# Performance work log

Measured on AMD Instinct MI355X. Metric: run time of the kernel, lower is better.

The kernel has to match this reference:

```python
import jax, jax.numpy as jnp
import numpy as np

NUM_HEADS = 16
WINDOW_SIZE = 256  # config.window_size; layer is 'local'


def setup_inputs() -> dict:
    key = jax.random.key(0)
    ks = jax.random.split(key, 8)
    B, S, H = 4, 2048, 1024
    scale = 1.0 / np.sqrt(H)
    return {
        "x": jax.random.normal(ks[0], (B, S, H), dtype=jnp.float32),
        "x_clean": jax.random.normal(ks[1], (B, S, H), dtype=jnp.float32),
        "ablation_mask": jax.random.uniform(ks[2], (B, S, H), dtype=jnp.float32),
        "Wq": jax.random.normal(ks[3], (H, H), dtype=jnp.float32) * scale,
        "Wk": jax.random.normal(ks[4], (H, H), dtype=jnp.float32) * scale,
        "Wv": jax.random.normal(ks[5], (H, H), dtype=jnp.float32) * scale,
        "Wo": jax.random.normal(ks[6], (H, H), dtype=jnp.float32) * scale,
        "bo": jnp.zeros((H,), dtype=jnp.float32),
    }


def reference(x, x_clean, ablation_mask, Wq, Wk, Wv, Wo, bo):
    B, S, H = x.shape
    nh, hd = NUM_HEADS, H // NUM_HEADS

    def proj(inp, W):  # torch Linear: inp @ W.T -> split heads -> [B, nh, S, hd]
        return jnp.einsum('bsh,oh->bso', inp, W).reshape(B, S, nh, hd).transpose(0, 2, 1, 3)

    q = proj(x, Wq)
    k = proj(x_clean, Wk)
    v = proj(x_clean, Wv)

    # NOTE: original applies NO 1/sqrt(head_dim) scaling.
    scores = jnp.einsum('bnsd,bntd->bnst', q, k)  # [B, nh, S, S]

    i = jnp.arange(S)[:, None]
    j = jnp.arange(S)[None, :]
    # local mask: forbid future (j > i) OR too-far past (j <= i - window)
    masked = (j > i) | (j <= i - WINDOW_SIZE)
    scores = jnp.where(masked[None, None, :, :], -jnp.inf, scores)

    attn = jax.nn.softmax(scores, axis=-1)
    context = jnp.einsum('bnst,bntd->bnsd', attn, v)          # [B, nh, S, hd]
    context = context.transpose(0, 2, 1, 3).reshape(B, S, H)   # merge heads
    context = context * ablation_mask
    return jnp.einsum('bsh,oh->bso', context, Wo) + bo
```

## Files before the change

### kernel.cpp

```cpp
#include <hip/hip_runtime.h>
#include <hip/hip_bf16.h>
#include <cstddef>

#define SB 4
#define SS 2048
#define SH 1024
#define NH 16
#define HD 64
#define WIN 256

typedef __attribute__((ext_vector_type(8))) short bf16x8;
typedef __attribute__((ext_vector_type(8))) _Float16 f16x8;
typedef __attribute__((ext_vector_type(2))) __fp16 fp16v2;
typedef __attribute__((ext_vector_type(4))) float f32x4;

static __device__ __forceinline__ ushort2 pk_bf16(float a, float b) {
    __hip_bfloat162 h = __float22bfloat162_rn(make_float2(a, b));
    union { __hip_bfloat162 h2; ushort2 u2; } u;
    u.h2 = h;
    return u.u2;
}
static __device__ __forceinline__ unsigned short pk1(float a) {
    return pk_bf16(a, 0.f).x;
}

static __device__ __forceinline__ void async16(const void* gptr, void* lptr) {
    __builtin_amdgcn_global_load_lds(
        (const __attribute__((address_space(1))) unsigned int*)gptr,
        (__attribute__((address_space(3))) unsigned int*)lptr, 16, 0, 0);
}

__global__ __launch_bounds__(256) void cvt_all(
    const float* __restrict__ x,  const float* __restrict__ xc,
    const float* __restrict__ Wq, const float* __restrict__ Wk,
    const float* __restrict__ Wv, const float* __restrict__ Wo,
    _Float16* __restrict__ xh,  _Float16* __restrict__ xch,
    _Float16* __restrict__ Wqh, _Float16* __restrict__ Wkh,
    _Float16* __restrict__ Wvh, _Float16* __restrict__ Woh)
{
    const int I4 = SB * SS * SH / 4;
    const int W4 = SH * SH / 4;
    int idx = blockIdx.x * 256 + threadIdx.x;
    const float* src;
    _Float16* dst;
    int off;
    if (idx < I4) { src = x; dst = xh; off = idx; }
    else if (idx < 2 * I4) { src = xc; dst = xch; off = idx - I4; }
    else {
        int r = idx - 2 * I4;
        int wi = r >> 18;
        off = r & (W4 - 1);
        src = (wi == 0) ? Wq : (wi == 1) ? Wk : (wi == 2) ? Wv : Wo;
        dst = (wi == 0) ? Wqh : (wi == 1) ? Wkh : (wi == 2) ? Wvh : Woh;
    }
    float4 v = ((const float4*)src)[off];
    union { fp16v2 h[2]; uint2 u; } t;
    t.h[0] = __builtin_amdgcn_cvt_pkrtz(v.x, v.y);
    t.h[1] = __builtin_amdgcn_cvt_pkrtz(v.z, v.w);
    ((uint2*)dst)[off] = t.u;
}

__global__ __launch_bounds__(256) void gemm_qkv(
    const _Float16* __restrict__ xh, const _Float16* __restrict__ xch,
    const _Float16* __restrict__ Wqh, const _Float16* __restrict__ Wkh,
    const _Float16* __restrict__ Wvh,
    _Float16* __restrict__ Qh, _Float16* __restrict__ Kh,
    unsigned short* __restrict__ Vt)
{
    const int M = SB * SS, N = SH, K = SH;
    __shared__ __align__(16) unsigned short smem[2 * 128 * 64];
    _Float16* Ah = (_Float16*)smem;
    _Float16* Bh = (_Float16*)smem + 8192;

    const int z = blockIdx.z;
    const _Float16* A = (z == 0) ? xh : xch;
    const _Float16* W = (z == 0) ? Wqh : (z == 1) ? Wkh : Wvh;

    const int tid = threadIdx.x;
    const int m0 = blockIdx.x * 128;
    const int n0 = blockIdx.y * 128;
    const int wave = tid >> 6;
    const int lane = tid & 63;
    const int wm = (wave & 1) * 64;
    const int wn = (wave >> 1) * 64;
    const int lrow = lane & 15;
    const int lk8 = (lane >> 4) * 8;
    const int rq = (lane >> 4) * 4;

    f32x4 acc[4][4];
#pragma unroll
    for (int i = 0; i < 4; ++i)
#pragma unroll
        for (int j = 0; j < 4; ++j)
            acc[i][j] = (f32x4){0.f, 0.f, 0.f, 0.f};

    for (int k0 = 0; k0 < K; k0 += 64) {
        __syncthreads();
#pragma unroll
        for (int ki = 0; ki < 2; ++ki)
#pragma unroll
            for (int u = 0; u < 2; ++u) {
                int reg = u * 4 + wave;
                int slot = reg * 64 + lane;
                int row = slot >> 2;
                int k8 = (slot & 3) * 8;
                async16(A + (size_t)(m0 + row) * K + k0 + ki * 32 + k8,
                        Ah + ki * 4096 + reg * 512);
                async16(W + (size_t)(n0 + row) * K + k0 + ki * 32 + k8,
                        Bh + ki * 4096 + reg * 512);
            }
        __syncthreads();

#pragma unroll
        for (int ki = 0; ki < 2; ++ki) {
            f16x8 bf[4];
#pragma unroll
            for (int j = 0; j < 4; ++j)
                bf[j] = *(const f16x8*)&Bh[ki * 4096 + (wn + j * 16 + lrow) * 32 + lk8];
#pragma unroll
            for (int i = 0; i < 4; ++i) {
                f16x8 af = *(const f16x8*)&Ah[ki * 4096 + (wm + i * 16 + lrow) * 32 + lk8];
#pragma unroll
                for (int j = 0; j < 4; ++j)
                    acc[i][j] = __builtin_amdgcn_mfma_f32_16x16x32_f16(af, bf[j], acc[i][j], 0, 0, 0);
            }
        }
    }

    if (z < 2) {
        _Float16* C = (z == 0) ? Qh : Kh;
#pragma unroll
        for (int i = 0; i < 4; ++i) {
            int rbase = m0 + wm + i * 16 + rq;
#pragma unroll
            for (int j = 0; j < 4; ++j) {
                int col = n0 + wn + j * 16 + lrow;
#pragma unroll
                for (int r = 0; r < 4; ++r)
                    C[(size_t)(rbase + r) * N + col] = (_Float16)acc[i][j][r];
            }
        }
    } else {
        unsigned short* T = smem;
#pragma unroll
        for (int p = 0; p < 2; ++p) {
            __syncthreads();
            if (wn == p * 64) {
#pragma unroll
                for (int i = 0; i < 4; ++i) {
                    int mloc = wm + i * 16 + rq;
#pragma unroll
                    for (int j = 0; j < 4; ++j) {
                        int cl = j * 16 + lrow;
                        *(ushort4*)&T[cl * 136 + mloc] = make_ushort4(
                            pk1(acc[i][j][0]), pk1(acc[i][j][1]),
                            pk1(acc[i][j][2]), pk1(acc[i][j][3]));
                    }
                }
            }
            __syncthreads();
#pragma unroll
            for (int u = 0; u < 4; ++u) {
                int slot = u * 256 + tid;
                int cl = slot >> 4;
                int m8 = (slot & 15) * 8;
                *(uint4*)(Vt + (size_t)(n0 + p * 64 + cl) * M + m0 + m8) =
                    *(const uint4*)&T[cl * 136 + m8];
            }
        }
    }
}

__global__ __launch_bounds__(256) void gemm_o(
    const _Float16* __restrict__ A, const _Float16* __restrict__ W,
    const float* __restrict__ bias, float* __restrict__ C)
{
    const int M = SB * SS, N = SH, K = SH;
    __shared__ __align__(16) unsigned short smem[2 * 128 * 64];
    _Float16* Ah = (_Float16*)smem;
    _Float16* Bh = (_Float16*)smem + 8192;

    const int tid = threadIdx.x;
    const int m0 = blockIdx.x * 128;
    const int n0 = blockIdx.y * 128;
    const int wave = tid >> 6;
    const int lane = tid & 63;
    const int wm = (wave & 1) * 64;
    const int wn = (wave >> 1) * 64;
    const int lrow = lane & 15;
    const int lk8 = (lane >> 4) * 8;
    const int rq = (lane >> 4) * 4;

    f32x4 acc[4][4];
#pragma unroll
    for (int i = 0; i < 4; ++i)
#pragma unroll
        for (int j = 0; j < 4; ++j)
            acc[i][j] = (f32x4){0.f, 0.f, 0.f, 0.f};

    for (int k0 = 0; k0 < K; k0 += 64) {
        __syncthreads();
#pragma unroll
        for (int ki = 0; ki < 2; ++ki)
#pragma unroll
            for (int u = 0; u < 2; ++u) {
                int reg = u * 4 + wave;
                int slot = reg * 64 + lane;
                int row = slot >> 2;
                int k8 = (slot & 3) * 8;
                async16(A + (size_t)(m0 + row) * K + k0 + ki * 32 + k8,
                        Ah + ki * 4096 + reg * 512);
                async16(W + (size_t)(n0 + row) * K + k0 + ki * 32 + k8,
                        Bh + ki * 4096 + reg * 512);
            }
        __syncthreads();

#pragma unroll
        for (int ki = 0; ki < 2; ++ki) {
            f16x8 bf[4];
#pragma unroll
            for (int j = 0; j < 4; ++j)
                bf[j] = *(const f16x8*)&Bh[ki * 4096 + (wn + j * 16 + lrow) * 32 + lk8];
#pragma unroll
            for (int i = 0; i < 4; ++i) {
                f16x8 af = *(const f16x8*)&Ah[ki * 4096 + (wm + i * 16 + lrow) * 32 + lk8];
#pragma unroll
                for (int j = 0; j < 4; ++j)
                    acc[i][j] = __builtin_amdgcn_mfma_f32_16x16x32_f16(af, bf[j], acc[i][j], 0, 0, 0);
            }
        }
    }

#pragma unroll
    for (int i = 0; i < 4; ++i) {
        int rbase = m0 + wm + i * 16 + rq;
#pragma unroll
        for (int j = 0; j < 4; ++j) {
            int col = n0 + wn + j * 16 + lrow;
            float badd = bias[col];
#pragma unroll
            for (int r = 0; r < 4; ++r)
                C[(size_t)(rbase + r) * N + col] = acc[i][j][r] + badd;
        }
    }
}

__global__ __launch_bounds__(256) void attn4(
    const _Float16* Qg, const _Float16* __restrict__ Kg,
    const unsigned short* __restrict__ Vtg, const float* __restrict__ amask,
    _Float16* ctxg)
{
    __shared__ __align__(16) _Float16 K_s[2][2 * 64 * 32];
    __shared__ __align__(16) unsigned short V_s[2][2 * 64 * 32];
    __shared__ __align__(16) unsigned short P_s[4][32 * 72];

    const int t = threadIdx.x;
    const int wave = t >> 6, lane = t & 63;
    const int qb = blockIdx.x, h = blockIdx.y, b = blockIdx.z;
    const int t0 = qb * 128;
    const int wq = t0 + wave * 32;
    const int lrow = lane & 15;
    const int lk8 = (lane >> 4) * 8;
    const int rq = (lane >> 4) * 4;
    const int M = SB * SS;
    unsigned short* P = P_s[wave];

    f16x8 qf[2][2];
#pragma unroll
    for (int i = 0; i < 2; ++i)
#pragma unroll
        for (int ki = 0; ki < 2; ++ki)
            qf[i][ki] = *(const f16x8*)(Qg +
                (size_t)(b * SS + wq + i * 16 + lrow) * SH + h * HD + ki * 32 + lk8);

    f32x4 o[2][4];
    float lsum[2][4];
#pragma unroll
    for (int i = 0; i < 2; ++i)
#pragma unroll
        for (int j = 0; j < 4; ++j) o[i][j] = (f32x4){0.f, 0.f, 0.f, 0.f};
#pragma unroll
    for (int i = 0; i < 2; ++i)
#pragma unroll
        for (int r = 0; r < 4; ++r) lsum[i][r] = 0.f;

    int cl0 = t0 - (WIN - 1);
    cl0 = cl0 < 0 ? 0 : cl0;
    const int c_lo = cl0 >> 6;
    const int c_hi = (t0 >> 6) + 1;

    auto stage = [&](int c, int buf) {
        const int key0 = c * 64;
#pragma unroll
        for (int ki = 0; ki < 2; ++ki) {
            int slot = wave * 64 + lane;
            int row = slot >> 2;
            int e8 = (slot & 3) * 8;
            async16(Kg + (size_t)(b * SS + key0 + row) * SH + h * HD + ki * 32 + e8,
                    (_Float16*)K_s[buf] + ki * 2048 + wave * 512);
            async16(Vtg + (size_t)(h * HD + row) * M + b * SS + key0 + ki * 32 + e8,
                    (unsigned short*)V_s[buf] + ki * 2048 + wave * 512);
        }
    };

    stage(c_lo, c_lo & 1);
    __syncthreads();

    for (int c = c_lo; c <= c_hi; ++c) {
        const int cur = c & 1;
        if (c < c_hi) stage(c + 1, cur ^ 1);
        const int key0 = c * 64;
        if (key0 <= wq + 31 && key0 + 63 >= wq - (WIN - 1)) {
            const _Float16* Kc = (const _Float16*)K_s[cur];
            const unsigned short* Vc = (const unsigned short*)V_s[cur];

            f32x4 s[2][4];
#pragma unroll
            for (int i = 0; i < 2; ++i)
#pragma unroll
                for (int j = 0; j < 4; ++j) s[i][j] = (f32x4){0.f, 0.f, 0.f, 0.f};
#pragma unroll
            for (int ki = 0; ki < 2; ++ki)
#pragma unroll
                for (int j = 0; j < 4; ++j) {
                    f16x8 bh = *(const f16x8*)&Kc[ki * 2048 + (j * 16 + lrow) * 32 + lk8];
#pragma unroll
                    for (int i = 0; i < 2; ++i)
                        s[i][j] = __builtin_amdgcn_mfma_f32_16x16x32_f16(qf[i][ki], bh, s[i][j], 0, 0, 0);
                }

#pragma unroll
            for (int i = 0; i < 2; ++i)
#pragma unroll
                for (int j = 0; j < 4; ++j) {
                    int jg = key0 + j * 16 + lrow;
#pragma unroll
                    for (int r = 0; r < 4; ++r) {
                        int qg = wq + i * 16 + rq + r;
                        float p = (jg <= qg && jg > qg - WIN) ? __expf(s[i][j][r]) : 0.f;
                        lsum[i][r] += p;
                        P[(i * 16 + rq + r) * 72 + j * 16 + lrow] = pk1(p);
                    }
                }

#pragma unroll
            for (int ki = 0; ki < 2; ++ki) {
                bf16x8 pf[2];
#pragma unroll
                for (int i = 0; i < 2; ++i)
                    pf[i] = *(const bf16x8*)&P[(i * 16 + lrow) * 72 + ki * 32 + lk8];
#pragma unroll
                for (int j = 0; j < 4; ++j) {
                    bf16x8 vf = *(const bf16x8*)&Vc[ki * 2048 + (j * 16 + lrow) * 32 + lk8];
#pragma unroll
                    for (int i = 0; i < 2; ++i)
                        o[i][j] = __builtin_amdgcn_mfma_f32_16x16x32_bf16(pf[i], vf, o[i][j], 0, 0, 0);
                }
            }
        }
        __syncthreads();
    }

#pragma unroll
    for (int i = 0; i < 2; ++i)
#pragma unroll
        for (int r = 0; r < 4; ++r) {
#pragma unroll
            for (int m = 1; m < 16; m <<= 1)
                lsum[i][r] += __shfl_xor(lsum[i][r], m);
        }

    _Float16* Pf = (_Float16*)P;
#pragma unroll
    for (int i = 0; i < 2; ++i)
#pragma unroll
        for (int r = 0; r < 4; ++r) {
            float inv = 1.f / lsum[i][r];
#pragma unroll
            for (int j = 0; j < 4; ++j)
                Pf[(i * 16 + rq + r) * 72 + j * 16 + lrow] = (_Float16)(o[i][j][r] * inv);
        }
#pragma unroll
    for (int u = 0; u < 4; ++u) {
        int slot = u * 64 + lane;
        int ro = slot >> 3;
        int d8 = (slot & 7) * 8;
        f16x8 v = *(const f16x8*)&Pf[ro * 72 + d8];
        size_t g = (size_t)(b * SS + wq + ro) * SH + h * HD + d8;
        float4 ma = *(const float4*)(amask + g);
        float4 mb = *(const float4*)(amask + g + 4);
        f16x8 rs;
        rs[0] = (_Float16)((float)v[0] * ma.x);
        rs[1] = (_Float16)((float)v[1] * ma.y);
        rs[2] = (_Float16)((float)v[2] * ma.z);
        rs[3] = (_Float16)((float)v[3] * ma.w);
        rs[4] = (_Float16)((float)v[4] * mb.x);
        rs[5] = (_Float16)((float)v[5] * mb.y);
        rs[6] = (_Float16)((float)v[6] * mb.z);
        rs[7] = (_Float16)((float)v[7] * mb.w);
        *(f16x8*)(ctxg + g) = rs;
    }
}

extern "C" void kernel_launch(void* const* d_in, const int* in_sizes, int n_in,
                              void* d_out, int out_size, void* d_ws, size_t ws_size,
                              hipStream_t stream)
{
    const float* x     = (const float*)d_in[0];
    const float* xc    = (const float*)d_in[1];
    const float* amask = (const float*)d_in[2];
    const float* Wq    = (const float*)d_in[3];
    const float* Wk    = (const float*)d_in[4];
    const float* Wv    = (const float*)d_in[5];
    const float* Wo    = (const float*)d_in[6];
    const float* bo    = (const float*)d_in[7];
    float* out = (float*)d_out;

    const int M = SB * SS;
    const size_t BUF = (size_t)M * SH;
    const size_t WBUF = (size_t)SH * SH;
    _Float16* xh  = (_Float16*)d_ws;
    _Float16* xch = xh + BUF;
    _Float16* Qh  = xch + BUF;
    _Float16* Kh  = Qh + BUF;
    unsigned short* Vt = (unsigned short*)(Kh + BUF);
    _Float16* Wqh = (_Float16*)(Vt + BUF);
    _Float16* Wkh = Wqh + WBUF;
    _Float16* Wvh = Wkh + WBUF;
    _Float16* Woh = Wvh + WBUF;
    _Float16* ctx = Qh;

    const int total4 = 2 * (M * SH / 4) + 4 * (SH * SH / 4);
    hipLaunchKernelGGL(cvt_all, dim3(total4 / 256), dim3(256), 0, stream,
                       x, xc, Wq, Wk, Wv, Wo, xh, xch, Wqh, Wkh, Wvh, Woh);

    hipLaunchKernelGGL(gemm_qkv, dim3(M / 128, SH / 128, 3), dim3(256), 0, stream,
                       xh, xch, Wqh, Wkh, Wvh, Qh, Kh, Vt);

    hipLaunchKernelGGL(attn4, dim3(SS / 128, NH, SB), dim3(256), 0, stream,
                       Qh, Kh, Vt, amask, ctx);

    hipLaunchKernelGGL(gemm_o, dim3(M / 128, SH / 128), dim3(256), 0, stream,
                       ctx, Woh, bo, out);
}
```

Baseline: 288.6 us.

## Stage Q/K GEMM output through LDS and widen attention blocks to 256 queries

The Q/K projection epilogue now writes the accumulators into an LDS tile and then stores them to global memory as coalesced 16-byte rows, replacing scattered 2-byte stores. The attention kernel moves to 512-thread blocks covering 256 queries, each with 8 waves, on a flattened 1D grid ordered so blocks with the same query tile across heads and batches launch together. Each staged K/V chunk is now shared by twice as many query rows, which cuts redundant window loads. In exchange each block loops over more chunks that some waves skip, and fewer blocks are launched.

Measured after the change: 276.8 us. 4.1% less time.

```diff
diff --git a/kernel.cpp b/kernel.cpp
--- a/kernel.cpp
+++ b/kernel.cpp
@@ -68,7 +68,7 @@
     unsigned short* __restrict__ Vt)
 {
     const int M = SB * SS, N = SH, K = SH;
-    __shared__ __align__(16) unsigned short smem[2 * 128 * 64];
+    __shared__ __align__(16) unsigned short smem[128 * 136];
     _Float16* Ah = (_Float16*)smem;
     _Float16* Bh = (_Float16*)smem + 8192;
 
@@ -129,16 +129,27 @@
 
     if (z < 2) {
         _Float16* C = (z == 0) ? Qh : Kh;
+        _Float16* T = (_Float16*)smem;
+        __syncthreads();
 #pragma unroll
         for (int i = 0; i < 4; ++i) {
-            int rbase = m0 + wm + i * 16 + rq;
+            int rloc = wm + i * 16 + rq;
 #pragma unroll
             for (int j = 0; j < 4; ++j) {
-                int col = n0 + wn + j * 16 + lrow;
+                int cl = wn + j * 16 + lrow;
 #pragma unroll
                 for (int r = 0; r < 4; ++r)
-                    C[(size_t)(rbase + r) * N + col] = (_Float16)acc[i][j][r];
-            }
+                    T[(rloc + r) * 136 + cl] = (_Float16)acc[i][j][r];
+            }
+        }
+        __syncthreads();
+#pragma unroll
+        for (int u = 0; u < 8; ++u) {
+            int slot = u * 256 + tid;
+            int row = slot >> 4;
+            int c8 = (slot & 15) * 8;
+            *(uint4*)(C + (size_t)(m0 + row) * N + n0 + c8) =
+                *(const uint4*)&T[row * 136 + c8];
         }
     } else {
         unsigned short* T = smem;
@@ -245,19 +256,22 @@
     }
 }
 
-__global__ __launch_bounds__(256) void attn4(
+__global__ __launch_bounds__(512, 4) void attn5(
     const _Float16* Qg, const _Float16* __restrict__ Kg,
     const unsigned short* __restrict__ Vtg, const float* __restrict__ amask,
     _Float16* ctxg)
 {
     __shared__ __align__(16) _Float16 K_s[2][2 * 64 * 32];
     __shared__ __align__(16) unsigned short V_s[2][2 * 64 * 32];
-    __shared__ __align__(16) unsigned short P_s[4][32 * 72];
+    __shared__ __align__(16) unsigned short P_s[8][32 * 72];
 
     const int t = threadIdx.x;
     const int wave = t >> 6, lane = t & 63;
-    const int qb = blockIdx.x, h = blockIdx.y, b = blockIdx.z;
-    const int t0 = qb * 128;
+    const int id = blockIdx.x;
+    const int qb = id >> 6;
+    const int pr = id & 63;
+    const int h = pr & 15, b = pr >> 4;
+    const int t0 = qb * 256;
     const int wq = t0 + wave * 32;
     const int lrow = lane & 15;
     const int lk8 = (lane >> 4) * 8;
@@ -265,6 +279,10 @@
     const int M = SB * SS;
     unsigned short* P = P_s[wave];
 
+    const int ski = t >> 8;
+    const int srow = (t & 255) >> 2;
+    const int se8 = (t & 3) * 8;
+
     f16x8 qf[2][2];
 #pragma unroll
     for (int i = 0; i < 2; ++i)
@@ -287,20 +305,14 @@
     int cl0 = t0 - (WIN - 1);
     cl0 = cl0 < 0 ? 0 : cl0;
     const int c_lo = cl0 >> 6;
-    const int c_hi = (t0 >> 6) + 1;
+    const int c_hi = (t0 >> 6) + 3;
 
     auto stage = [&](int c, int buf) {
         const int key0 = c * 64;
-#pragma unroll
-        for (int ki = 0; ki < 2; ++ki) {
-            int slot = wave * 64 + lane;
-            int row = slot >> 2;
-            int e8 = (slot & 3) * 8;
-            async16(Kg + (size_t)(b * SS + key0 + row) * SH + h * HD + ki * 32 + e8,
-                    (_Float16*)K_s[buf] + ki * 2048 + wave * 512);
-            async16(Vtg + (size_t)(h * HD + row) * M + b * SS + key0 + ki * 32 + e8,
-                    (unsigned short*)V_s[buf] + ki * 2048 + wave * 512);
-        }
+        async16(Kg + (size_t)(b * SS + key0 + srow) * SH + h * HD + ski * 32 + se8,
+                (_Float16*)K_s[buf] + wave * 512);
+        async16(Vtg + (size_t)(h * HD + srow) * M + b * SS + key0 + ski * 32 + se8,
+                (unsigned short*)V_s[buf] + wave * 512);
     };
 
     stage(c_lo, c_lo & 1);
@@ -437,7 +449,7 @@
     hipLaunchKernelGGL(gemm_qkv, dim3(M / 128, SH / 128, 3), dim3(256), 0, stream,
                        xh, xch, Wqh, Wkh, Wvh, Qh, Kh, Vt);
 
-    hipLaunchKernelGGL(attn4, dim3(SS / 128, NH, SB), dim3(256), 0, stream,
+    hipLaunchKernelGGL(attn5, dim3((SS / 256) * NH * SB), dim3(512), 0, stream,
                        Qh, Kh, Vt, amask, ctx);
 
     hipLaunchKernelGGL(gemm_o, dim3(M / 128, SH / 128), dim3(256), 0, stream,
```
